# Kernel optimization log

Hardware: AMD Instinct MI355X
Metric: run time of the kernel (lower is better)

## Reference

```python
import jax, jax.numpy as jnp
import numpy as np

N_SUB, N_AGR, N_URB = 200000, 400000, 200000
H, OUT = 64, 6
E_SS, E_AS, E_US = 2000000, 4000000, 2000000
NLAYERS = 3


def setup_inputs() -> dict:
    key = jax.random.key(0)
    ks = jax.random.split(key, 12)
    s = 0.05
    return {
        "x_sub": jax.random.normal(ks[0], (N_SUB, H), jnp.float32),
        "x_agr": jax.random.normal(ks[1], (N_AGR, H), jnp.float32),
        "x_urb": jax.random.normal(ks[2], (N_URB, H), jnp.float32),
        # stacked SAGEConv params: [layer, relation(ss,as,us), ...]
        "Wl": jax.random.normal(ks[3], (NLAYERS, 3, H, H), jnp.float32) * s,
        "bl": jax.random.normal(ks[4], (NLAYERS, 3, H), jnp.float32) * s,
        "Wr": jax.random.normal(ks[5], (NLAYERS, 3, H, H), jnp.float32) * s,
        "Wf": jax.random.normal(ks[6], (OUT, H), jnp.float32) * s,
        "bf": jnp.zeros((OUT,), jnp.float32),
        "edge_ss": jax.random.randint(ks[7], (2, E_SS), 0, N_SUB, jnp.int32),
        "edge_as_src": jax.random.randint(ks[8], (E_AS,), 0, N_AGR, jnp.int32),
        "edge_as_dst": jax.random.randint(ks[9], (E_AS,), 0, N_SUB, jnp.int32),
        "edge_us": jax.random.randint(ks[10], (2, E_US), 0, N_SUB, jnp.int32),
    }


def _sage(x_src, x_dst, src, dst, Wl, b, Wr, n_dst, mean):
    # PyG SAGEConv: lin_l(aggr_j x_j) + lin_r(x_i); lin_r has no bias
    msg = x_src[src]                                   # [E, d_src] gather
    agg = jax.ops.segment_sum(msg, dst, num_segments=n_dst)
    if mean:  # static python flag
        deg = jax.ops.segment_sum(jnp.ones((src.shape[0], 1), x_src.dtype),
                                  dst, num_segments=n_dst)
        agg = agg / jnp.maximum(deg, 1.0)
    return agg @ Wl.T + b + x_dst @ Wr.T


def reference(x_sub, x_agr, x_urb, Wl, bl, Wr, Wf, bf,
              edge_ss, edge_as_src, edge_as_dst, edge_us):
    sub = x_sub
    for i in range(NLAYERS):
        mean_ss = i > 0  # layer-0 sub->sub uses aggr='sum', later layers PyG default 'mean'
        h = _sage(sub, sub, edge_ss[0], edge_ss[1], Wl[i, 0], bl[i, 0], Wr[i, 0], N_SUB, mean_ss)
        h = h + _sage(x_agr, sub, edge_as_src, edge_as_dst, Wl[i, 1], bl[i, 1], Wr[i, 1], N_SUB, False)
        h = h + _sage(x_urb, sub, edge_us[0], edge_us[1], Wl[i, 2], bl[i, 2], Wr[i, 2], N_SUB, False)
        sub = jax.nn.relu(h)  # Identity norm (batch_norm=False), dropout is eval-mode identity
        # x_dict['agr'] / x_dict['urb'] reset to skip features -> agr/urb convs never affect output
    return jax.nn.softmax(sub @ Wf.T + bf, axis=1)
```

## Files before the change

### kernel.cpp

```cpp
#include <hip/hip_runtime.h>
#include <cstdio>
#include <cstdint>


#define NSUB 200000
#define NAGR 400000
#define NURB 200000
#define HDIM 64
#define ESS 2000000
#define EAS 4000000
#define EUS 2000000
#define NB 512
#define CAP_AS 8608
#define CAP_SS 4320
#define CAP_US 4320
#define CHUNK 4096
#define NCH_AS 977
#define NCH_SS 489
#define NCH_US 489
#define CDIV(a,b) (((a)+(b)-1)/(b))

using u16 = unsigned short;
typedef __attribute__((ext_vector_type(8))) short v8s;
typedef __attribute__((ext_vector_type(4))) float v4f;

__device__ __forceinline__ float bu2f(u16 u){
  union { unsigned int i; float f; } c; c.i = ((unsigned int)u) << 16; return c.f;
}
__device__ __forceinline__ u16 f2bu(float x){
  union { float f; unsigned int i; } c; c.f = x;
  unsigned int r = c.i + 0x7fffu + ((c.i >> 16) & 1u);
  return (u16)(r >> 16);
}
__device__ __forceinline__ int bucket_of(int d){
  return (int)(((unsigned long long)(unsigned)d * NB) / NSUB);
}
__device__ __forceinline__ int bucket_base(int b){
  return (int)(((unsigned long long)b * NSUB + NB - 1) / NB);
}

__global__ void kcast(const float4* __restrict__ in, uint2* __restrict__ outp, int n4){
  int i = blockIdx.x*256 + threadIdx.x;
  if(i<n4){
    float4 v = in[i];
    uint2 o;
    o.x = (unsigned int)f2bu(v.x) | ((unsigned int)f2bu(v.y)<<16);
    o.y = (unsigned int)f2bu(v.z) | ((unsigned int)f2bu(v.w)<<16);
    outp[i]=o;
  }
}

__global__ void kcast2(const float4* __restrict__ a, uint2* __restrict__ oa, int n4a,
                       const float4* __restrict__ u, uint2* __restrict__ ou, int n4u){
  int i = blockIdx.x*256 + threadIdx.x;
  const float4* src; uint2* dst; int idx;
  if(i < n4a){ src=a; dst=oa; idx=i; }
  else { idx = i - n4a; if(idx >= n4u) return; src=u; dst=ou; }
  float4 v = src[idx];
  uint2 o;
  o.x = (unsigned int)f2bu(v.x) | ((unsigned int)f2bu(v.y)<<16);
  o.y = (unsigned int)f2bu(v.z) | ((unsigned int)f2bu(v.w)<<16);
  dst[idx]=o;
}

__global__ void kprep(const float* __restrict__ Wl, const float* __restrict__ Wr,
                      const float* __restrict__ bl, u16* __restrict__ Wg,
                      float* __restrict__ bsum, int* __restrict__ gcur){
  int l = blockIdx.x, tid = threadIdx.x;
  for(int i=tid; i<16384; i+=256){
    int o = i>>8, k = i&255, a = k>>6, kk = k&63;
    float v;
    if(a<3) v = Wl[(((size_t)l*3+a)*64+o)*64+kk];
    else    v = Wr[(((size_t)l*3+0)*64+o)*64+kk]
              + Wr[(((size_t)l*3+1)*64+o)*64+kk]
              + Wr[(((size_t)l*3+2)*64+o)*64+kk];
    Wg[((size_t)l*64+o)*256 + k] = f2bu(v);
  }
  if(tid<64) bsum[l*64+tid] = bl[(l*3+0)*64+tid] + bl[(l*3+1)*64+tid] + bl[(l*3+2)*64+tid];
  for(int i=tid;i<NB;i+=256) gcur[l*NB+i]=0;
}

__global__ __launch_bounds__(256) void kpart(
    const int* __restrict__ e_ss, const int* __restrict__ e_as_s,
    const int* __restrict__ e_as_d, const int* __restrict__ e_us,
    unsigned* __restrict__ pAS, unsigned* __restrict__ pSS,
    unsigned* __restrict__ pUS, int* __restrict__ gcur){
  __shared__ int cnt[NB];
  __shared__ int seg[NB];
  int bid = blockIdx.x, tid = threadIdx.x;
  int rel, chunk, cap, Erel;
  const int *sp, *dp; unsigned* part;
  if(bid < NCH_AS){ rel=0; chunk=bid; sp=e_as_s; dp=e_as_d; part=pAS; cap=CAP_AS; Erel=EAS; }
  else if(bid < NCH_AS+NCH_SS){ rel=1; chunk=bid-NCH_AS; sp=e_ss; dp=e_ss+ESS; part=pSS; cap=CAP_SS; Erel=ESS; }
  else { rel=2; chunk=bid-NCH_AS-NCH_SS; sp=e_us; dp=e_us+EUS; part=pUS; cap=CAP_US; Erel=EUS; }
  int m = Erel - chunk*CHUNK; if(m>CHUNK) m=CHUNK;
  for(int i=tid;i<NB;i+=256) cnt[i]=0;
  __syncthreads();
  unsigned pk[16], meta[16];
  #pragma unroll
  for(int j=0;j<16;j++){
    int idx = j*256+tid;
    meta[j] = 0xFFFFFFFFu;
    if(idx < m){
      long i = (long)chunk*CHUNK + idx;
      int s = sp[i], d = dp[i];
      int b = bucket_of(d);
      int r = atomicAdd(&cnt[b],1);
      pk[j] = ((unsigned)s<<9) | (unsigned)(d - bucket_base(b));
      meta[j] = ((unsigned)b<<16) | (unsigned)r;
    }
  }
  __syncthreads();
  for(int q=tid;q<NB;q+=256){
    int c = cnt[q];
    seg[q] = c ? atomicAdd(&gcur[rel*NB+q], c) : 0;
  }
  __syncthreads();
  #pragma unroll
  for(int j=0;j<16;j++){
    if(meta[j]!=0xFFFFFFFFu){
      int b = meta[j]>>16, r = meta[j]&0xFFFF;
      int pos = seg[b] + r;
      if(pos < cap) part[(long)b*cap + pos] = pk[j];
    }
  }
}

__global__ void kbscan(const int* __restrict__ gcur, int* __restrict__ boff){
  __shared__ int s1[256];
  int t = threadIdx.x;
  for(int rel=0; rel<3; rel++){
    int cap = (rel==0)?CAP_AS:((rel==1)?CAP_SS:CAP_US);
    int g0 = gcur[rel*NB + 2*t], g1 = gcur[rel*NB + 2*t+1];
    int a0 = g0<cap?g0:cap, a1 = g1<cap?g1:cap;
    s1[t] = a0+a1;
    __syncthreads();
    for(int off=1; off<256; off<<=1){
      int x = s1[t];
      int y = (t>=off)?s1[t-off]:0;
      __syncthreads();
      s1[t] = x+y;
      __syncthreads();
    }
    int e2 = s1[t]-(a0+a1);
    boff[rel*NB + 2*t]   = e2;
    boff[rel*NB + 2*t+1] = e2+a0;
    __syncthreads();
  }
}

__global__ __launch_bounds__(256) void ksort(
    const unsigned* __restrict__ pAS, const unsigned* __restrict__ pSS,
    const unsigned* __restrict__ pUS, const int* __restrict__ gcur,
    const int* __restrict__ boff,
    int* __restrict__ colAS, int* __restrict__ colSS, int* __restrict__ colUS,
    int* __restrict__ rpAS, int* __restrict__ rpSS, int* __restrict__ rpUS,
    int* __restrict__ degAS, int* __restrict__ degSS, int* __restrict__ degUS){
  __shared__ int degl[512];
  __shared__ int excl[512];
  __shared__ int cur[512];
  __shared__ int s1[256];
  int bid = blockIdx.x;
  int rel = bid >> 9, b = bid & 511;
  const unsigned* part; int cap; int* col; int* rp; int* deg;
  if(rel==0){ part=pAS; cap=CAP_AS; col=colAS; rp=rpAS; deg=degAS; }
  else if(rel==1){ part=pSS; cap=CAP_SS; col=colSS; rp=rpSS; deg=degSS; }
  else { part=pUS; cap=CAP_US; col=colUS; rp=rpUS; deg=degUS; }
  int tid = threadIdx.x;
  int base_b = bucket_base(b);
  int base_n = (b+1==NB)?NSUB:bucket_base(b+1);
  int width = base_n - base_b;
  int size = gcur[rel*NB+b]; if(size>cap) size=cap;
  int bo = boff[rel*NB+b];
  const unsigned* pb = part + (long)b*cap;
  degl[tid]=0; degl[256+tid]=0;
  __syncthreads();
  for(int i=tid;i<size;i+=256) atomicAdd(&degl[pb[i]&511u],1);
  __syncthreads();
  int a0=degl[2*tid], a1=degl[2*tid+1];
  s1[tid]=a0+a1;
  __syncthreads();
  for(int off=1; off<256; off<<=1){
    int x=s1[tid];
    int y=(tid>=off)?s1[tid-off]:0;
    __syncthreads();
    s1[tid]=x+y;
    __syncthreads();
  }
  int e2 = s1[tid]-(a0+a1);
  excl[2*tid]=e2;     excl[2*tid+1]=e2+a0;
  cur[2*tid]=e2;      cur[2*tid+1]=e2+a0;
  __syncthreads();
  for(int n=tid;n<width;n+=256){
    rp[base_b+n]  = bo + excl[n];
    deg[base_b+n] = degl[n];
  }
  for(int i=tid;i<size;i+=256){
    unsigned p = pb[i];
    int dl = (int)(p&511u);
    int r = atomicAdd(&cur[dl],1);
    col[bo + r] = (int)(p>>9);
  }
}

__device__ __forceinline__ float gather1(const float* x, size_t idx){ return x[idx]; }
__device__ __forceinline__ float gather1(const u16* x, size_t idx){ return bu2f(x[idx]); }

template<typename T, bool MEAN>
__device__ __forceinline__ void agg_one(const T* __restrict__ x,
    const int* __restrict__ rowptr, const int* __restrict__ deg,
    const int* __restrict__ col, u16* __restrict__ out, int w, int lane){
  int s = __builtin_amdgcn_readfirstlane(rowptr[w]);
  int d = __builtin_amdgcn_readfirstlane(deg[w]);
  float acc = 0.f;
  int i=0;
  for(; i+8<=d; i+=8){
    int sj[8];
    #pragma unroll
    for(int j=0;j<8;j++) sj[j]=col[s+i+j];
    float a[8];
    #pragma unroll
    for(int j=0;j<8;j++) a[j]=gather1(x,(size_t)sj[j]*HDIM+lane);
    acc += ((a[0]+a[1])+(a[2]+a[3])) + ((a[4]+a[5])+(a[6]+a[7]));
  }
  for(; i<d; i++) acc += gather1(x,(size_t)col[s+i]*HDIM+lane);
  float sc = 1.f;
  if(MEAN) sc = 1.f/(float)(d>1?d:1);
  out[(size_t)w*HDIM + lane] = f2bu(acc*sc);
}

template<typename T, bool MEAN>
__global__ void kaggregate(const T* __restrict__ x, const int* __restrict__ rowptr,
                           const int* __restrict__ deg, const int* __restrict__ col,
                           u16* __restrict__ out, int ndst){
  int gid = blockIdx.x*256 + threadIdx.x;
  int w = gid>>6, lane = gid&63;
  if(w>=ndst) return;
  agg_one<T,MEAN>(x, rowptr, deg, col, out, w, lane);
}

template<typename T>
__global__ void kaggAU(const T* __restrict__ xa, const int* __restrict__ rpA,
                       const int* __restrict__ degA, const int* __restrict__ colA,
                       u16* __restrict__ outA,
                       const T* __restrict__ xu, const int* __restrict__ rpU,
                       const int* __restrict__ degU, const int* __restrict__ colU,
                       u16* __restrict__ outU){
  int gid = blockIdx.x*256 + threadIdx.x;
  int w = gid>>6, lane = gid&63;
  if(w < NSUB)        agg_one<T,false>(xa, rpA, degA, colA, outA, w, lane);
  else if(w < 2*NSUB) agg_one<T,false>(xu, rpU, degU, colU, outU, w-NSUB, lane);
}

__global__ __launch_bounds__(256) void kgemmM(
    const u16* __restrict__ aggSS, const u16* __restrict__ aggAS,
    const u16* __restrict__ aggUS, const u16* __restrict__ subIn,
    const u16* __restrict__ Wg, const float* __restrict__ bsum,
    u16* __restrict__ subOut){
  __shared__ u16 ldsW[64*264];
  __shared__ float ldsB[64];
  int tid = threadIdx.x;
  const unsigned* wg32 = (const unsigned*)Wg;
  for(int i=tid; i<8192; i+=256){
    int o = i>>7, k2 = i&127;
    ((unsigned*)ldsW)[o*132 + k2] = wg32[i];
  }
  if(tid<64) ldsB[tid] = bsum[tid];
  __syncthreads();
  int lane = tid&63, wid = tid>>6;
  long row0 = (long)blockIdx.x*64 + wid*16;
  const u16* arrs[4] = {aggSS, aggAS, aggUS, subIn};
  v4f acc[4] = {};
  long rowl = row0 + (lane&15);
  int kq = (lane>>4)*8;
  #pragma unroll
  for(int s=0;s<8;s++){
    const u16* ap = arrs[s>>1] + rowl*64 + (s&1)*32 + kq;
    v8s a = *(const v8s*)ap;
    #pragma unroll
    for(int t=0;t<4;t++){
      v8s bf = *(const v8s*)&ldsW[(t*16+(lane&15))*264 + s*32 + kq];
      acc[t] = __builtin_amdgcn_mfma_f32_16x16x32_bf16(a, bf, acc[t], 0,0,0);
    }
  }
  int m0 = (lane>>4)*4;
  #pragma unroll
  for(int t=0;t<4;t++){
    int o = t*16 + (lane&15);
    float bb = ldsB[o];
    #pragma unroll
    for(int r=0;r<4;r++){
      float h = acc[t][r] + bb;
      h = fmaxf(h, 0.f);
      subOut[(row0 + m0 + r)*64 + o] = f2bu(h);
    }
  }
}

__global__ void khead(const u16* __restrict__ sub, const float* __restrict__ Wf,
                      const float* __restrict__ bfv, float* __restrict__ out, int n){
  __shared__ float w[6*64];
  __shared__ float b[6];
  for(int j=threadIdx.x; j<384; j+=256) w[j]=Wf[j];
  if(threadIdx.x<6) b[threadIdx.x]=bfv[threadIdx.x];
  __syncthreads();
  int i = blockIdx.x*256 + threadIdx.x;
  if(i>=n) return;
  const unsigned int* row = (const unsigned int*)(sub + (size_t)i*HDIM);
  float d0=b[0],d1=b[1],d2=b[2],d3=b[3],d4=b[4],d5=b[5];
  #pragma unroll 8
  for(int k2=0;k2<32;k2++){
    unsigned int v = row[k2];
    float lo = bu2f((u16)(v&0xffffu));
    float hi = bu2f((u16)(v>>16));
    int k = 2*k2;
    d0 += lo*w[0*64+k] + hi*w[0*64+k+1];
    d1 += lo*w[1*64+k] + hi*w[1*64+k+1];
    d2 += lo*w[2*64+k] + hi*w[2*64+k+1];
    d3 += lo*w[3*64+k] + hi*w[3*64+k+1];
    d4 += lo*w[4*64+k] + hi*w[4*64+k+1];
    d5 += lo*w[5*64+k] + hi*w[5*64+k+1];
  }
  float m = fmaxf(fmaxf(fmaxf(d0,d1),fmaxf(d2,d3)),fmaxf(d4,d5));
  float e0=expf(d0-m), e1=expf(d1-m), e2=expf(d2-m);
  float e3=expf(d3-m), e4=expf(d4-m), e5=expf(d5-m);
  float inv = 1.0f/(e0+e1+e2+e3+e4+e5);
  float2* op = (float2*)(out + (size_t)i*6);
  float2 r0; r0.x=e0*inv; r0.y=e1*inv;
  float2 r1; r1.x=e2*inv; r1.y=e3*inv;
  float2 r2; r2.x=e4*inv; r2.y=e5*inv;
  op[0]=r0; op[1]=r1; op[2]=r2;
}

extern "C" void kernel_launch(void* const* d_in, const int* in_sizes, int n_in,
                              void* d_out, int out_size, void* d_ws, size_t ws_size,
                              hipStream_t stream) {
  const float* x_sub = (const float*)d_in[0];
  const float* x_agr = (const float*)d_in[1];
  const float* x_urb = (const float*)d_in[2];
  const float* Wl    = (const float*)d_in[3];
  const float* bl    = (const float*)d_in[4];
  const float* Wr    = (const float*)d_in[5];
  const float* Wf    = (const float*)d_in[6];
  const float* bfv   = (const float*)d_in[7];
  const int* e_ss    = (const int*)d_in[8];
  const int* e_as_s  = (const int*)d_in[9];
  const int* e_as_d  = (const int*)d_in[10];
  const int* e_us    = (const int*)d_in[11];
  float* out = (float*)d_out;

  char* ws = (char*)d_ws;
  size_t off = 0;
  auto alloc = [&](size_t bytes)->void*{
    void* p = ws + off; off += (bytes + 255) & ~(size_t)255; return p;
  };
  u16*  subA   = (u16*) alloc((size_t)NSUB*HDIM*2);
  u16*  subB   = (u16*) alloc((size_t)NSUB*HDIM*2);
  u16*  aggSS  = (u16*) alloc((size_t)NSUB*HDIM*2);
  u16*  aggAS  = (u16*) alloc((size_t)NSUB*HDIM*2);
  u16*  aggUS  = (u16*) alloc((size_t)NSUB*HDIM*2);
  int*  colAS  = (int*)  alloc((size_t)EAS*4);
  int*  colSS  = (int*)  alloc((size_t)ESS*4);
  int*  colUS  = (int*)  alloc((size_t)EUS*4);
  int*  rpAS   = (int*)  alloc((size_t)NSUB*4);
  int*  rpSS   = (int*)  alloc((size_t)NSUB*4);
  int*  rpUS   = (int*)  alloc((size_t)NSUB*4);
  int*  degAS  = (int*)  alloc((size_t)NSUB*4);
  int*  degSS  = (int*)  alloc((size_t)NSUB*4);
  int*  degUS  = (int*)  alloc((size_t)NSUB*4);
  int*  gcur   = (int*)  alloc((size_t)3*NB*4);
  int*  boff   = (int*)  alloc((size_t)3*NB*4);
  u16*  Wg     = (u16*)  alloc((size_t)3*64*256*2);
  float* bsum  = (float*)alloc((size_t)3*64*4);
  size_t off0 = off;
  unsigned* pAS = (unsigned*)alloc((size_t)NB*CAP_AS*4);
  unsigned* pSS = (unsigned*)alloc((size_t)NB*CAP_SS*4);
  unsigned* pUS = (unsigned*)alloc((size_t)NB*CAP_US*4);
  size_t end_part = off;
  u16* agr16 = (u16*)(ws + off0);
  u16* urb16 = agr16 + (size_t)NAGR*HDIM;
  size_t end_cast = off0 + ((size_t)NAGR+NURB)*HDIM*2;
  size_t need_full = end_part > end_cast ? end_part : end_cast;
  bool bf16_gather = (ws_size >= need_full);
  if(ws_size < end_part){
    fprintf(stderr, "kernel_launch: ws too small: need %zu have %zu\n", end_part, ws_size);
    return;
  }

  kcast<<<CDIV(NSUB*HDIM/4,256),256,0,stream>>>((const float4*)x_sub, (uint2*)subA, NSUB*HDIM/4);
  kprep<<<3,256,0,stream>>>(Wl, Wr, bl, Wg, bsum, gcur);

  kpart<<<NCH_AS+NCH_SS+NCH_US,256,0,stream>>>(e_ss, e_as_s, e_as_d, e_us,
                                               pAS, pSS, pUS, gcur);
  kbscan<<<1,256,0,stream>>>(gcur, boff);
  ksort<<<3*NB,256,0,stream>>>(pAS, pSS, pUS, gcur, boff,
                               colAS, colSS, colUS,
                               rpAS, rpSS, rpUS,
                               degAS, degSS, degUS);

  const int auBlocks = CDIV(2*NSUB*64,256);
  if(bf16_gather){
    int n4a = NAGR*HDIM/4, n4u = NURB*HDIM/4;
    kcast2<<<CDIV(n4a+n4u,256),256,0,stream>>>((const float4*)x_agr, (uint2*)agr16, n4a,
                                               (const float4*)x_urb, (uint2*)urb16, n4u);
    kaggAU<u16><<<auBlocks,256,0,stream>>>(agr16, rpAS, degAS, colAS, aggAS,
                                           urb16, rpUS, degUS, colUS, aggUS);
  } else {
    kaggAU<float><<<auBlocks,256,0,stream>>>(x_agr, rpAS, degAS, colAS, aggAS,
                                             x_urb, rpUS, degUS, colUS, aggUS);
  }

  const int aggBlocks = CDIV(NSUB*64,256);
  const int gemmBlocks = NSUB/64;
  kaggregate<u16,false><<<aggBlocks,256,0,stream>>>(subA, rpSS, degSS, colSS, aggSS, NSUB);
  kgemmM<<<gemmBlocks,256,0,stream>>>(aggSS, aggAS, aggUS, subA, Wg + 0*16384, bsum + 0*64, subB);
  kaggregate<u16,true><<<aggBlocks,256,0,stream>>>(subB, rpSS, degSS, colSS, aggSS, NSUB);
  kgemmM<<<gemmBlocks,256,0,stream>>>(aggSS, aggAS, aggUS, subB, Wg + 1*16384, bsum + 1*64, subA);
  kaggregate<u16,true><<<aggBlocks,256,0,stream>>>(subA, rpSS, degSS, colSS, aggSS, NSUB);
  kgemmM<<<gemmBlocks,256,0,stream>>>(aggSS, aggAS, aggUS, subA, Wg + 2*16384, bsum + 2*64, subB);

  khead<<<CDIV(NSUB,256),256,0,stream>>>(subB, Wf, bfv, out, NSUB);
}
```

Before: 915.2 us.

## Gather bf16 rows with 16-byte vector loads, two destinations per wavefront

Replaces the one-lane-per-feature bf16 gather with a scheme where each wavefront handles two destination nodes. Each 8-lane group loads a full 128-byte row via 16-byte vector loads, covering 4 edges per group, and partial sums are reduced with shuffles. Out-of-range edges are redirected to a zero padding row appended to each feature table, and the col arrays get slack so reads past the end stay in bounds. The aim is fewer, wider memory transactions and higher memory-level parallelism per wave, at the cost of divergence when the two nodes' degrees differ and of extra shuffle work.

Measured after the change: 756.8 us. 17.3% less time.

```diff
diff --git a/kernel.cpp b/kernel.cpp
--- a/kernel.cpp
+++ b/kernel.cpp
@@ -18,11 +18,14 @@
 #define NCH_AS 977
 #define NCH_SS 489
 #define NCH_US 489
+#define COL_SLACK 16384
 #define CDIV(a,b) (((a)+(b)-1)/(b))
 
 using u16 = unsigned short;
 typedef __attribute__((ext_vector_type(8))) short v8s;
 typedef __attribute__((ext_vector_type(4))) float v4f;
+typedef __attribute__((ext_vector_type(2))) float v2f;
+typedef __attribute__((ext_vector_type(4))) unsigned int v4u;
 
 __device__ __forceinline__ float bu2f(u16 u){
   union { unsigned int i; float f; } c; c.i = ((unsigned int)u) << 16; return c.f;
@@ -53,19 +56,31 @@
 __global__ void kcast2(const float4* __restrict__ a, uint2* __restrict__ oa, int n4a,
                        const float4* __restrict__ u, uint2* __restrict__ ou, int n4u){
   int i = blockIdx.x*256 + threadIdx.x;
-  const float4* src; uint2* dst; int idx;
-  if(i < n4a){ src=a; dst=oa; idx=i; }
-  else { idx = i - n4a; if(idx >= n4u) return; src=u; dst=ou; }
-  float4 v = src[idx];
-  uint2 o;
-  o.x = (unsigned int)f2bu(v.x) | ((unsigned int)f2bu(v.y)<<16);
-  o.y = (unsigned int)f2bu(v.z) | ((unsigned int)f2bu(v.w)<<16);
-  dst[idx]=o;
+  if(i < n4a){
+    float4 v = a[i];
+    uint2 o;
+    o.x = (unsigned int)f2bu(v.x) | ((unsigned int)f2bu(v.y)<<16);
+    o.y = (unsigned int)f2bu(v.z) | ((unsigned int)f2bu(v.w)<<16);
+    oa[i]=o;
+  } else if(i < n4a + n4u){
+    int idx = i - n4a;
+    float4 v = u[idx];
+    uint2 o;
+    o.x = (unsigned int)f2bu(v.x) | ((unsigned int)f2bu(v.y)<<16);
+    o.y = (unsigned int)f2bu(v.z) | ((unsigned int)f2bu(v.w)<<16);
+    ou[idx]=o;
+  } else {
+    int k = i - n4a - n4u;
+    uint2 z; z.x=0u; z.y=0u;
+    if(k < 16) oa[(size_t)n4a + k] = z;
+    else if(k < 32) ou[(size_t)n4u + (k-16)] = z;
+  }
 }
 
 __global__ void kprep(const float* __restrict__ Wl, const float* __restrict__ Wr,
                       const float* __restrict__ bl, u16* __restrict__ Wg,
-                      float* __restrict__ bsum, int* __restrict__ gcur){
+                      float* __restrict__ bsum, int* __restrict__ gcur,
+                      u16* __restrict__ zA, u16* __restrict__ zB){
   int l = blockIdx.x, tid = threadIdx.x;
   for(int i=tid; i<16384; i+=256){
     int o = i>>8, k = i&255, a = k>>6, kk = k&63;
@@ -78,6 +93,11 @@
   }
   if(tid<64) bsum[l*64+tid] = bl[(l*3+0)*64+tid] + bl[(l*3+1)*64+tid] + bl[(l*3+2)*64+tid];
   for(int i=tid;i<NB;i+=256) gcur[l*NB+i]=0;
+  if(l==0){
+    uint2 z; z.x=0u; z.y=0u;
+    if(tid<16)          ((uint2*)(zA + (size_t)NSUB*HDIM))[tid]    = z;
+    else if(tid<32)     ((uint2*)(zB + (size_t)NSUB*HDIM))[tid-16] = z;
+  }
 }
 
 __global__ __launch_bounds__(256) void kpart(
@@ -204,10 +224,9 @@
 }
 
 __device__ __forceinline__ float gather1(const float* x, size_t idx){ return x[idx]; }
-__device__ __forceinline__ float gather1(const u16* x, size_t idx){ return bu2f(x[idx]); }
-
-template<typename T, bool MEAN>
-__device__ __forceinline__ void agg_one(const T* __restrict__ x,
+
+template<bool MEAN>
+__device__ __forceinline__ void agg_one_f32(const float* __restrict__ x,
     const int* __restrict__ rowptr, const int* __restrict__ deg,
     const int* __restrict__ col, u16* __restrict__ out, int w, int lane){
   int s = __builtin_amdgcn_readfirstlane(rowptr[w]);
@@ -229,27 +248,104 @@
   out[(size_t)w*HDIM + lane] = f2bu(acc*sc);
 }
 
-template<typename T, bool MEAN>
-__global__ void kaggregate(const T* __restrict__ x, const int* __restrict__ rowptr,
-                           const int* __restrict__ deg, const int* __restrict__ col,
-                           u16* __restrict__ out, int ndst){
+__global__ __launch_bounds__(256) void kaggAUf(
+    const float* __restrict__ xa, const int* __restrict__ rpA,
+    const int* __restrict__ degA, const int* __restrict__ colA,
+    u16* __restrict__ outA,
+    const float* __restrict__ xu, const int* __restrict__ rpU,
+    const int* __restrict__ degU, const int* __restrict__ colU,
+    u16* __restrict__ outU){
   int gid = blockIdx.x*256 + threadIdx.x;
   int w = gid>>6, lane = gid&63;
-  if(w>=ndst) return;
-  agg_one<T,MEAN>(x, rowptr, deg, col, out, w, lane);
-}
-
-template<typename T>
-__global__ void kaggAU(const T* __restrict__ xa, const int* __restrict__ rpA,
-                       const int* __restrict__ degA, const int* __restrict__ colA,
-                       u16* __restrict__ outA,
-                       const T* __restrict__ xu, const int* __restrict__ rpU,
-                       const int* __restrict__ degU, const int* __restrict__ colU,
-                       u16* __restrict__ outU){
+  if(w < NSUB)        agg_one_f32<false>(xa, rpA, degA, colA, outA, w, lane);
+  else if(w < 2*NSUB) agg_one_f32<false>(xu, rpU, degU, colU, outU, w-NSUB, lane);
+}
+
+template<bool MEAN>
+__device__ __forceinline__ void agg_pair(const u16* __restrict__ x,
+    const int* __restrict__ rowptr, const int* __restrict__ deg,
+    const int* __restrict__ col, u16* __restrict__ out,
+    int w0, int lane, int zrow){
+  int h  = lane>>5;
+  int gl = (lane>>3)&3;
+  int q  = lane&7;
+  int w  = w0 + h;
+  int s  = rowptr[w];
+  int d  = deg[w];
+  int d0 = __builtin_amdgcn_readlane(d, 0);
+  int d1 = __builtin_amdgcn_readlane(d, 32);
+  int dm = d0 > d1 ? d0 : d1;
+  const u16* xq = x + ((unsigned)q<<3);
+  v2f acc[4];
+  #pragma unroll
+  for(int k=0;k<4;k++){ acc[k].x=0.f; acc[k].y=0.f; }
+  for(int i=0; i<dm; i+=16){
+    int eb = i + gl;
+    const int* cp = col + (s + eb);
+    int cj[4];
+    #pragma unroll
+    for(int j=0;j<4;j++){
+      int c = cp[j*4];
+      cj[j] = (eb + j*4 < d) ? c : zrow;
+    }
+    v8s vv[4];
+    #pragma unroll
+    for(int j=0;j<4;j++)
+      vv[j] = *(const v8s*)(xq + (size_t)(unsigned)cj[j]*HDIM);
+    #pragma unroll
+    for(int j=0;j<4;j++){
+      v4u dw = __builtin_bit_cast(v4u, vv[j]);
+      #pragma unroll
+      for(int k=0;k<4;k++){
+        unsigned v = dw[k];
+        v2f p;
+        p.x = __uint_as_float(v << 16);
+        p.y = __uint_as_float(v & 0xffff0000u);
+        acc[k] += p;
+      }
+    }
+  }
+  #pragma unroll
+  for(int k=0;k<4;k++){
+    v2f v = acc[k];
+    v2f t;
+    t.x = __shfl_xor(v.x, 8);  t.y = __shfl_xor(v.y, 8);  v += t;
+    t.x = __shfl_xor(v.x, 16); t.y = __shfl_xor(v.y, 16); v += t;
+    acc[k] = v;
+  }
+  float sc = 1.f;
+  if(MEAN) sc = 1.f/(float)(d>1?d:1);
+  if(gl==0){
+    v4u r;
+    #pragma unroll
+    for(int k=0;k<4;k++)
+      r[k] = (unsigned)f2bu(acc[k].x*sc) | ((unsigned)f2bu(acc[k].y*sc)<<16);
+    *(v4u*)(out + (size_t)w*HDIM + ((unsigned)q<<3)) = r;
+  }
+}
+
+template<bool MEAN>
+__global__ __launch_bounds__(256) void kaggP(
+    const u16* __restrict__ x, const int* __restrict__ rowptr,
+    const int* __restrict__ deg, const int* __restrict__ col,
+    u16* __restrict__ out, int npair, int zrow){
   int gid = blockIdx.x*256 + threadIdx.x;
-  int w = gid>>6, lane = gid&63;
-  if(w < NSUB)        agg_one<T,false>(xa, rpA, degA, colA, outA, w, lane);
-  else if(w < 2*NSUB) agg_one<T,false>(xu, rpU, degU, colU, outU, w-NSUB, lane);
+  int p = gid>>6, lane = gid&63;
+  if(p>=npair) return;
+  agg_pair<MEAN>(x, rowptr, deg, col, out, 2*p, lane, zrow);
+}
+
+__global__ __launch_bounds__(256) void kaggAUP(
+    const u16* __restrict__ xa, const int* __restrict__ rpA,
+    const int* __restrict__ degA, const int* __restrict__ colA,
+    u16* __restrict__ outA,
+    const u16* __restrict__ xu, const int* __restrict__ rpU,
+    const int* __restrict__ degU, const int* __restrict__ colU,
+    u16* __restrict__ outU){
+  int gid = blockIdx.x*256 + threadIdx.x;
+  int p = gid>>6, lane = gid&63;
+  if(p < NSUB/2)      agg_pair<false>(xa, rpA, degA, colA, outA, 2*p, lane, NAGR);
+  else if(p < NSUB)   agg_pair<false>(xu, rpU, degU, colU, outU, 2*(p-NSUB/2), lane, NURB);
 }
 
 __global__ __launch_bounds__(256) void kgemmM(
@@ -354,14 +450,14 @@
   auto alloc = [&](size_t bytes)->void*{
     void* p = ws + off; off += (bytes + 255) & ~(size_t)255; return p;
   };
-  u16*  subA   = (u16*) alloc((size_t)NSUB*HDIM*2);
-  u16*  subB   = (u16*) alloc((size_t)NSUB*HDIM*2);
+  u16*  subA   = (u16*) alloc((size_t)(NSUB+1)*HDIM*2);
+  u16*  subB   = (u16*) alloc((size_t)(NSUB+1)*HDIM*2);
   u16*  aggSS  = (u16*) alloc((size_t)NSUB*HDIM*2);
   u16*  aggAS  = (u16*) alloc((size_t)NSUB*HDIM*2);
   u16*  aggUS  = (u16*) alloc((size_t)NSUB*HDIM*2);
-  int*  colAS  = (int*)  alloc((size_t)EAS*4);
-  int*  colSS  = (int*)  alloc((size_t)ESS*4);
-  int*  colUS  = (int*)  alloc((size_t)EUS*4);
+  int*  colAS  = (int*)  alloc((size_t)(EAS+COL_SLACK)*4);
+  int*  colSS  = (int*)  alloc((size_t)(ESS+COL_SLACK)*4);
+  int*  colUS  = (int*)  alloc((size_t)(EUS+COL_SLACK)*4);
   int*  rpAS   = (int*)  alloc((size_t)NSUB*4);
   int*  rpSS   = (int*)  alloc((size_t)NSUB*4);
   int*  rpUS   = (int*)  alloc((size_t)NSUB*4);
@@ -378,8 +474,8 @@
   unsigned* pUS = (unsigned*)alloc((size_t)NB*CAP_US*4);
   size_t end_part = off;
   u16* agr16 = (u16*)(ws + off0);
-  u16* urb16 = agr16 + (size_t)NAGR*HDIM;
-  size_t end_cast = off0 + ((size_t)NAGR+NURB)*HDIM*2;
+  u16* urb16 = agr16 + (size_t)(NAGR+1)*HDIM;
+  size_t end_cast = off0 + ((size_t)NAGR+NURB+2)*HDIM*2;
   size_t need_full = end_part > end_cast ? end_part : end_cast;
   bool bf16_gather = (ws_size >= need_full);
   if(ws_size < end_part){
@@ -388,7 +484,7 @@
   }
 
   kcast<<<CDIV(NSUB*HDIM/4,256),256,0,stream>>>((const float4*)x_sub, (uint2*)subA, NSUB*HDIM/4);
-  kprep<<<3,256,0,stream>>>(Wl, Wr, bl, Wg, bsum, gcur);
+  kprep<<<3,256,0,stream>>>(Wl, Wr, bl, Wg, bsum, gcur, subA, subB);
 
   kpart<<<NCH_AS+NCH_SS+NCH_US,256,0,stream>>>(e_ss, e_as_s, e_as_d, e_us,
                                                pAS, pSS, pUS, gcur);
@@ -398,25 +494,24 @@
                                rpAS, rpSS, rpUS,
                                degAS, degSS, degUS);
 
-  const int auBlocks = CDIV(2*NSUB*64,256);
   if(bf16_gather){
     int n4a = NAGR*HDIM/4, n4u = NURB*HDIM/4;
-    kcast2<<<CDIV(n4a+n4u,256),256,0,stream>>>((const float4*)x_agr, (uint2*)agr16, n4a,
-                                               (const float4*)x_urb, (uint2*)urb16, n4u);
-    kaggAU<u16><<<auBlocks,256,0,stream>>>(agr16, rpAS, degAS, colAS, aggAS,
-                                           urb16, rpUS, degUS, colUS, aggUS);
+    kcast2<<<CDIV(n4a+n4u+32,256),256,0,stream>>>((const float4*)x_agr, (uint2*)agr16, n4a,
+                                                  (const float4*)x_urb, (uint2*)urb16, n4u);
+    kaggAUP<<<NSUB*64/256,256,0,stream>>>(agr16, rpAS, degAS, colAS, aggAS,
+                                          urb16, rpUS, degUS, colUS, aggUS);
   } else {
-    kaggAU<float><<<auBlocks,256,0,stream>>>(x_agr, rpAS, degAS, colAS, aggAS,
-                                             x_urb, rpUS, degUS, colUS, aggUS);
-  }
-
-  const int aggBlocks = CDIV(NSUB*64,256);
+    kaggAUf<<<CDIV(2*NSUB*64,256),256,0,stream>>>(x_agr, rpAS, degAS, colAS, aggAS,
+                                                  x_urb, rpUS, degUS, colUS, aggUS);
+  }
+
+  const int pairBlocks = (NSUB/2)*64/256;
   const int gemmBlocks = NSUB/64;
-  kaggregate<u16,false><<<aggBlocks,256,0,stream>>>(subA, rpSS, degSS, colSS, aggSS, NSUB);
+  kaggP<false><<<pairBlocks,256,0,stream>>>(subA, rpSS, degSS, colSS, aggSS, NSUB/2, NSUB);
   kgemmM<<<gemmBlocks,256,0,stream>>>(aggSS, aggAS, aggUS, subA, Wg + 0*16384, bsum + 0*64, subB);
-  kaggregate<u16,true><<<aggBlocks,256,0,stream>>>(subB, rpSS, degSS, colSS, aggSS, NSUB);
+  kaggP<true><<<pairBlocks,256,0,stream>>>(subB, rpSS, degSS, colSS, aggSS, NSUB/2, NSUB);
   kgemmM<<<gemmBlocks,256,0,stream>>>(aggSS, aggAS, aggUS, subB, Wg + 1*16384, bsum + 1*64, subA);
-  kaggregate<u16,true><<<aggBlocks,256,0,stream>>>(subA, rpSS, degSS, colSS, aggSS, NSUB);
+  kaggP<true><<<pairBlocks,256,0,stream>>>(subA, rpSS, degSS, colSS, aggSS, NSUB/2, NSUB);
   kgemmM<<<gemmBlocks,256,0,stream>>>(aggSS, aggAS, aggUS, subA, Wg + 2*16384, bsum + 2*64, subB);
 
   khead<<<CDIV(NSUB,256),256,0,stream>>>(subB, Wf, bfv, out, NSUB);
```
